# Kernel tuning notes

Hardware: AMD Instinct MI355X
Metric: run time of the kernel (lower is better)

## Reference

```python
import jax, jax.numpy as jnp
import numpy as np

D_MODEL = 1024
N_HEADS = 16
D_HEAD = D_MODEL // N_HEADS
BATCH = 2
SEQ = 2048


def setup_inputs() -> dict:
    key = jax.random.key(0)
    ks = jax.random.split(key, 16)
    s = 0.02
    d = D_MODEL
    return {
        "x": jax.random.normal(ks[0], (BATCH, SEQ, d), jnp.float32),
        "Wq": jax.random.normal(ks[1], (d, d), jnp.float32) * s,
        "bq": jnp.zeros((d,), jnp.float32),
        "Wk": jax.random.normal(ks[2], (d, d), jnp.float32) * s,
        "bk": jnp.zeros((d,), jnp.float32),
        "Wv": jax.random.normal(ks[3], (d, d), jnp.float32) * s,
        "bv": jnp.zeros((d,), jnp.float32),
        "Wo": jax.random.normal(ks[4], (d, d), jnp.float32) * s,
        "bo": jnp.zeros((d,), jnp.float32),
        "Wt": jax.random.normal(ks[5], (d, 1), jnp.float32) * s,
        "bt": jnp.zeros((1,), jnp.float32),
        "Wg": jax.random.normal(ks[6], (d, d), jnp.float32) * s,
        "bg": jnp.zeros((d,), jnp.float32),
    }


def _evolved_attention(x, Wq, bq, Wk, bk, Wv, bv, Wo, bo, Wt, bt, Wg, bg):
    B, S, D = x.shape
    H, dh = N_HEADS, D_HEAD

    def heads(y):  # [B,S,D] -> [B,H,S,dh]
        return y.reshape(B, S, H, dh).transpose(0, 2, 1, 3)

    q = heads(x @ Wq + bq)
    k = heads(x @ Wk + bk)
    v = heads(x @ Wv + bv)

    # cosine similarity (F.normalize with eps=1e-12)
    qn = q / jnp.maximum(jnp.linalg.norm(q, axis=-1, keepdims=True), 1e-12)
    kn = k / jnp.maximum(jnp.linalg.norm(k, axis=-1, keepdims=True), 1e-12)
    scores = jnp.einsum("bhqd,bhkd->bhqk", qn, kn)

    # adaptive temperature: sigmoid(temp_proj(mean_s x)) + 0.5, shape [B,1]
    temp = jax.nn.sigmoid(x.mean(axis=1) @ Wt + bt) + 0.5  # [B,1]
    scores = scores / temp[:, None, None, :]  # broadcast [B,1,1,1]

    # sparsemax-style: softmax over top-k (k = S//4), scattered back
    kk = max(1, S // 4)
    vals, idx = jax.lax.top_k(scores, kk)          # [B,H,S,kk]
    w = jax.nn.softmax(vals, axis=-1)
    rows = jnp.arange(B * H * S)[:, None]
    attn = (
        jnp.zeros((B * H * S, S), scores.dtype)
        .at[rows, idx.reshape(-1, kk)]
        .set(w.reshape(-1, kk))
        .reshape(B, H, S, S)
    )

    out = jnp.einsum("bhqk,bhkd->bhqd", attn, v)
    out = out.transpose(0, 2, 1, 3).reshape(B, S, D)
    out = out @ Wo + bo

    # highway gating
    gate = jax.nn.sigmoid(x @ Wg + bg)
    return gate * out + (1.0 - gate) * x


def reference(x, Wq, bq, Wk, bk, Wv, bv, Wo, bo, Wt, bt, Wg, bg):
    return _evolved_attention(x, Wq, bq, Wk, bk, Wv, bv, Wo, bo, Wt, bt, Wg, bg)
```

## Files before the change

### kernel.cpp

```cpp
#include <hip/hip_runtime.h>

typedef unsigned short u16;
typedef __attribute__((ext_vector_type(4))) float f32x4;
typedef __attribute__((ext_vector_type(8))) short bf16x8;
typedef __attribute__((ext_vector_type(4))) int i32x4;

#define BB 2
#define SS 2048
#define DD 1024
#define HH 16
#define DH 64
#define KK 512

#define OFF_SCAL  ((size_t)0)
#define OFF_WT    ((size_t)256)
#define OFF_XB    (OFF_WT + (size_t)5*1024*1024*2)
#define OFF_AO    OFF_XB
#define OFF_QH    (OFF_XB + (size_t)4096*1024*2)
#define OFF_QN    (OFF_QH + (size_t)4096*4096*2)
#define OFF_KN    (OFF_QN + (size_t)4096*1024*2)
#define OFF_VT    (OFF_KN + (size_t)4096*1024*2)

__device__ __forceinline__ float b2f(u16 u) { return __uint_as_float(((unsigned)u) << 16); }
__device__ __forceinline__ u16 f2b(float f) {
    unsigned u = __float_as_uint(f);
    return (u16)((u + 0x7fffu + ((u >> 16) & 1u)) >> 16);
}

__device__ __forceinline__ void gload16(const u16* g, u16* l) {
    __builtin_amdgcn_global_load_lds(
        (__attribute__((address_space(1))) void*)g,
        (__attribute__((address_space(3))) void*)l, 16, 0, 0);
}

__global__ __launch_bounds__(256) void convert_x(const float* x, u16* xb) {
    int i = (blockIdx.x * 256 + threadIdx.x) * 4;
    float4 v = *(const float4*)(x + i);
    u16 r0 = f2b(v.x), r1 = f2b(v.y), r2 = f2b(v.z), r3 = f2b(v.w);
    xb[i] = r0; xb[i + 1] = r1; xb[i + 2] = r2; xb[i + 3] = r3;
}

__global__ __launch_bounds__(256) void transpose_w(
        const float* Wq, const float* Wk, const float* Wv, const float* Wg, const float* Wo,
        u16* WT) {
    int z = blockIdx.z;
    const float* src = (z == 0) ? Wq : (z == 1) ? Wk : (z == 2) ? Wv : (z == 3) ? Wg : Wo;
    u16* dst = WT + (size_t)z * 1024 * 1024;
    __shared__ float tile[64][65];
    int n0 = blockIdx.x * 64, k0 = blockIdx.y * 64;
    int rbase = threadIdx.x >> 6, c = threadIdx.x & 63;
#pragma unroll
    for (int i = 0; i < 16; i++) {
        int r = i * 4 + rbase;
        tile[r][c] = src[(size_t)(k0 + r) * 1024 + n0 + c];
    }
    __syncthreads();
#pragma unroll
    for (int i = 0; i < 16; i++) {
        int r = i * 4 + rbase;
        dst[(size_t)(n0 + r) * 1024 + k0 + c] = f2b(tile[c][r]);
    }
}

__global__ __launch_bounds__(256) void temp_partial(const float* x, const float* Wt,
                                                    float* accbuf) {
    int b = blockIdx.x >> 5, ch = blockIdx.x & 31;
    float a = 0.f;
    for (int si = 0; si < 64; si++) {
        int s = ch * 64 + si;
        const float* xr = x + ((size_t)(b * SS + s)) * DD;
#pragma unroll
        for (int k = 0; k < 4; k++) {
            int c = threadIdx.x + k * 256;
            a += xr[c] * Wt[c];
        }
    }
    for (int o = 32; o; o >>= 1) a += __shfl_xor(a, o);
    __shared__ float red[4];
    if ((threadIdx.x & 63) == 0) red[threadIdx.x >> 6] = a;
    __syncthreads();
    if (threadIdx.x == 0) atomicAdd(&accbuf[b], red[0] + red[1] + red[2] + red[3]);
}

__global__ void temp_final(const float* accbuf, const float* bt, float* itemp) {
    int t = threadIdx.x;
    if (t < BB) {
        float v = accbuf[t] / (float)SS + bt[0];
        float tmp = 1.f / (1.f + __expf(-v)) + 0.5f;
        itemp[t] = 1.f / tmp;
    }
}

__global__ __launch_bounds__(256) void gemm_qkvg(
        const u16* X, const u16* WT,
        const float* bq, const float* bk, const float* bv, const float* bg, u16* Qh) {
    __shared__ __align__(16) u16 la[128 * 32];
    __shared__ __align__(16) u16 lb[128 * 32];
    int tid = threadIdx.x, wid = tid >> 6, lane = tid & 63;
    int quad = lane >> 4, ml = lane & 15;
    int m0 = blockIdx.x * 128, n0 = blockIdx.y * 128;
    int wr = wid >> 1, wc = wid & 1;

    f32x4 acc[4][4];
#pragma unroll
    for (int i = 0; i < 4; i++)
#pragma unroll
        for (int j = 0; j < 4; j++) acc[i][j] = (f32x4){0.f, 0.f, 0.f, 0.f};

    int t0 = wid * 2, t1 = t0 + 1;
    int r0 = lane >> 2, kp = lane & 3;
    const u16* ga0 = X + (size_t)(m0 + t0 * 16 + r0) * 1024 + kp * 8;
    const u16* ga1 = X + (size_t)(m0 + t1 * 16 + r0) * 1024 + kp * 8;
    const u16* gb0 = WT + (size_t)(n0 + t0 * 16 + r0) * 1024 + kp * 8;
    const u16* gb1 = WT + (size_t)(n0 + t1 * 16 + r0) * 1024 + kp * 8;
    u16* la0 = la + t0 * 512; u16* la1 = la + t1 * 512;
    u16* lb0 = lb + t0 * 512; u16* lb1 = lb + t1 * 512;

    for (int k0 = 0; k0 < 1024; k0 += 32) {
        gload16(ga0 + k0, la0);
        gload16(ga1 + k0, la1);
        gload16(gb0 + k0, lb0);
        gload16(gb1 + k0, lb1);
        __syncthreads();
        bf16x8 af[4], bfr[4];
#pragma unroll
        for (int mi = 0; mi < 4; mi++)
            af[mi] = *(const bf16x8*)&la[(wr * 64 + mi * 16 + ml) * 32 + quad * 8];
#pragma unroll
        for (int ni = 0; ni < 4; ni++)
            bfr[ni] = *(const bf16x8*)&lb[(wc * 64 + ni * 16 + ml) * 32 + quad * 8];
#pragma unroll
        for (int mi = 0; mi < 4; mi++)
#pragma unroll
            for (int ni = 0; ni < 4; ni++)
                acc[mi][ni] = __builtin_amdgcn_mfma_f32_16x16x32_bf16(af[mi], bfr[ni],
                                                                      acc[mi][ni], 0, 0, 0);
        __syncthreads();
    }

#pragma unroll
    for (int mi = 0; mi < 4; mi++)
#pragma unroll
        for (int ni = 0; ni < 4; ni++) {
            int col = n0 + wc * 64 + ni * 16 + ml;
            int mat = col >> 10, bc = col & 1023;
            const float* bp = (mat == 0) ? bq : (mat == 1) ? bk : (mat == 2) ? bv : bg;
            float bias = bp[bc];
#pragma unroll
            for (int r = 0; r < 4; r++) {
                int row = m0 + wr * 64 + mi * 16 + quad * 4 + r;
                Qh[(size_t)row * 4096 + col] = f2b(acc[mi][ni][r] + bias);
            }
        }
}

__global__ __launch_bounds__(256) void norm_repack(const u16* Qh, u16* qn, u16* kn, u16* vt) {
    int wid = threadIdx.x >> 6, lane = threadIdx.x & 63;
    int idx = blockIdx.x * 4 + wid;
    int token = idx >> 4, h = idx & 15;
    int b = token >> 11, s = token & 2047;
    int bh = b * HH + h;
    const u16* rowp = Qh + (size_t)token * 4096 + h * 64;
    float q = b2f(rowp[lane]);
    float k = b2f(rowp[1024 + lane]);
    u16 v = rowp[2048 + lane];
    float sq = q * q, sk = k * k;
    for (int o = 32; o; o >>= 1) { sq += __shfl_xor(sq, o); sk += __shfl_xor(sk, o); }
    float qd = fmaxf(sqrtf(sq), 1e-12f), kd = fmaxf(sqrtf(sk), 1e-12f);
    qn[((size_t)bh * SS + s) * DH + lane] = f2b(q / qd);
    kn[((size_t)bh * SS + s) * DH + lane] = f2b(k / kd);
    vt[((size_t)bh * DH + lane) * SS + s] = v;
}

#define EST 2088

__global__ __launch_bounds__(1024, 8) void attn_kernel(
        const u16* qn, const u16* kn, const u16* vt, const float* itemp, u16* ao) {
    __shared__ __align__(16) u16 e16[16 * EST];
    __shared__ float pvp[3][16][66];
    __shared__ float zrow_s[16];

    int tid = threadIdx.x, wid = tid >> 6, lane = tid & 63;
    int quad = lane >> 4, nl = lane & 15;
    int bid = blockIdx.x;
    int swz = (bid & 7) * 512 + (bid >> 3);
    int bh = swz >> 7, qt = swz & 127;
    int b = bh >> 4, h = bh & 15;
    const u16* qbase = qn + ((size_t)bh * SS + qt * 16) * DH;
    const u16* kbase = kn + (size_t)bh * SS * DH;
    const u16* vbase = vt + (size_t)bh * DH * SS;
    float it = itemp[b];

    bf16x8 aq0 = *(const bf16x8*)(qbase + nl * DH + quad * 8);
    bf16x8 aq1 = *(const bf16x8*)(qbase + nl * DH + 32 + quad * 8);

#pragma unroll 4
    for (int c = 0; c < 8; c++) {
        int j = c * 256 + wid * 16 + nl;
        const u16* kr = kbase + (size_t)j * DH;
        bf16x8 b0 = *(const bf16x8*)(kr + quad * 8);
        bf16x8 b1 = *(const bf16x8*)(kr + 32 + quad * 8);
        f32x4 acc = (f32x4){0.f, 0.f, 0.f, 0.f};
        __builtin_amdgcn_s_setprio(1);
        acc = __builtin_amdgcn_mfma_f32_16x16x32_bf16(aq0, b0, acc, 0, 0, 0);
        acc = __builtin_amdgcn_mfma_f32_16x16x32_bf16(aq1, b1, acc, 0, 0, 0);
        __builtin_amdgcn_s_setprio(0);
#pragma unroll
        for (int r = 0; r < 4; r++) e16[(quad * 4 + r) * EST + j] = f2b(acc[r] * it);
    }
    __syncthreads();

    {
        u16* rp = &e16[wid * EST];
        int kk[32];
#pragma unroll
        for (int i = 0; i < 4; i++) {
            i32x4 kv = *(const i32x4*)(rp + i * 512 + lane * 8);
#pragma unroll
            for (int j = 0; j < 4; j++) {
                unsigned r2 = (unsigned)kv[j];
                unsigned t = ((r2 >> 15) & 0x00010001u) * 0x7FFFu;
                unsigned key2 = r2 ^ 0x80008000u ^ t;
                int lo = (int)(key2 & 0xFFFFu), hi = (int)(key2 >> 16);
                asm volatile("v_mov_b32 %0, %1" : "=v"(kk[i * 8 + j * 2]) : "v"(lo));
                asm volatile("v_mov_b32 %0, %1" : "=v"(kk[i * 8 + j * 2 + 1]) : "v"(hi));
            }
        }

        int P = 0;
        for (int bit = 15; bit >= 0; bit--) {
            int cand = P | (1 << bit);
            int c0 = 0, c1 = 0, c2 = 0, c3 = 0;
#pragma unroll
            for (int c = 0; c < 32; c += 4) {
                c0 += (int)__popcll(__ballot(kk[c] >= cand));
                c1 += (int)__popcll(__ballot(kk[c + 1] >= cand));
                c2 += (int)__popcll(__ballot(kk[c + 2] >= cand));
                c3 += (int)__popcll(__ballot(kk[c + 3] >= cand));
            }
            int cnt = (c0 + c1) + (c2 + c3);
            if (cnt >= KK) P = cand;
            if (cnt == KK) break;
        }

        float z = 0.f;
#pragma unroll
        for (int i = 0; i < 4; i++) {
            i32x4 ev;
#pragma unroll
            for (int j = 0; j < 4; j++) {
                int k0i = kk[i * 8 + j * 2], k1i = kk[i * 8 + j * 2 + 1];
                unsigned r0 = (unsigned)k0i ^ ((k0i & 0x8000) ? 0x8000u : 0xFFFFu);
                unsigned r1 = (unsigned)k1i ^ ((k1i & 0x8000) ? 0x8000u : 0xFFFFu);
                float f0 = __uint_as_float(r0 << 16);
                float f1 = __uint_as_float(r1 << 16);
                float e0 = (k0i >= P) ? __expf(f0) : 0.f;
                float e1 = (k1i >= P) ? __expf(f1) : 0.f;
                z += e0 + e1;
                int pw;
                asm("v_cvt_pk_bf16_f32 %0, %1, %2" : "=v"(pw) : "v"(e0), "v"(e1));
                ev[j] = pw;
            }
            *(i32x4*)(rp + i * 512 + lane * 8) = ev;
        }
#pragma unroll
        for (int o = 32; o; o >>= 1) z += __shfl_xor(z, o);
        if (lane == 0) zrow_s[wid] = z;
    }
    __syncthreads();

    f32x4 accp = (f32x4){0.f, 0.f, 0.f, 0.f};
    int kq = wid >> 2, g = wid & 3;
    int dh = g * 16 + nl;
    const u16* vrow = vbase + (size_t)dh * SS;
#pragma unroll 4
    for (int c = 0; c < 8; c++) {
        int j0 = kq * 512 + c * 64;
#pragma unroll
        for (int ks = 0; ks < 2; ks++) {
            bf16x8 a = *(const bf16x8*)&e16[nl * EST + j0 + ks * 32 + quad * 8];
            bf16x8 bfr = *(const bf16x8*)(vrow + j0 + ks * 32 + quad * 8);
            __builtin_amdgcn_s_setprio(1);
            accp = __builtin_amdgcn_mfma_f32_16x16x32_bf16(a, bfr, accp, 0, 0, 0);
            __builtin_amdgcn_s_setprio(0);
        }
    }
    if (kq) {
#pragma unroll
        for (int r = 0; r < 4; r++) pvp[kq - 1][quad * 4 + r][dh] = accp[r];
    }
    __syncthreads();
    if (kq == 0) {
#pragma unroll
        for (int r = 0; r < 4; r++) {
            int q = quad * 4 + r;
            float val = (accp[r] + pvp[0][q][dh] + pvp[1][q][dh] + pvp[2][q][dh]) / zrow_s[q];
            size_t row = (size_t)(b * SS + qt * 16 + q);
            ao[row * DD + h * 64 + dh] = f2b(val);
        }
    }
}

__global__ __launch_bounds__(256) void gemm_out(
        const u16* AO, const u16* WTo, const float* bo,
        const u16* Qh, const float* x, float* out) {
    __shared__ __align__(16) u16 la[128 * 32];
    __shared__ __align__(16) u16 lb[128 * 32];
    int tid = threadIdx.x, wid = tid >> 6, lane = tid & 63;
    int quad = lane >> 4, ml = lane & 15;
    int m0 = blockIdx.x * 128, n0 = blockIdx.y * 128;
    int wr = wid >> 1, wc = wid & 1;

    f32x4 acc[4][4];
#pragma unroll
    for (int i = 0; i < 4; i++)
#pragma unroll
        for (int j = 0; j < 4; j++) acc[i][j] = (f32x4){0.f, 0.f, 0.f, 0.f};

    int t0 = wid * 2, t1 = t0 + 1;
    int r0 = lane >> 2, kp = lane & 3;
    const u16* ga0 = AO + (size_t)(m0 + t0 * 16 + r0) * 1024 + kp * 8;
    const u16* ga1 = AO + (size_t)(m0 + t1 * 16 + r0) * 1024 + kp * 8;
    const u16* gb0 = WTo + (size_t)(n0 + t0 * 16 + r0) * 1024 + kp * 8;
    const u16* gb1 = WTo + (size_t)(n0 + t1 * 16 + r0) * 1024 + kp * 8;
    u16* la0 = la + t0 * 512; u16* la1 = la + t1 * 512;
    u16* lb0 = lb + t0 * 512; u16* lb1 = lb + t1 * 512;

    for (int k0 = 0; k0 < 1024; k0 += 32) {
        gload16(ga0 + k0, la0);
        gload16(ga1 + k0, la1);
        gload16(gb0 + k0, lb0);
        gload16(gb1 + k0, lb1);
        __syncthreads();
        bf16x8 af[4], bfr[4];
#pragma unroll
        for (int mi = 0; mi < 4; mi++)
            af[mi] = *(const bf16x8*)&la[(wr * 64 + mi * 16 + ml) * 32 + quad * 8];
#pragma unroll
        for (int ni = 0; ni < 4; ni++)
            bfr[ni] = *(const bf16x8*)&lb[(wc * 64 + ni * 16 + ml) * 32 + quad * 8];
#pragma unroll
        for (int mi = 0; mi < 4; mi++)
#pragma unroll
            for (int ni = 0; ni < 4; ni++)
                acc[mi][ni] = __builtin_amdgcn_mfma_f32_16x16x32_bf16(af[mi], bfr[ni],
                                                                      acc[mi][ni], 0, 0, 0);
        __syncthreads();
    }

#pragma unroll
    for (int mi = 0; mi < 4; mi++)
#pragma unroll
        for (int ni = 0; ni < 4; ni++) {
            int col = n0 + wc * 64 + ni * 16 + ml;
            float bias = bo[col];
#pragma unroll
            for (int r = 0; r < 4; r++) {
                int row = m0 + wr * 64 + mi * 16 + quad * 4 + r;
                float gv = b2f(Qh[(size_t)row * 4096 + 3072 + col]);
                float gate = 1.f / (1.f + __expf(-gv));
                float xv = x[(size_t)row * 1024 + col];
                float o = acc[mi][ni][r] + bias;
                out[(size_t)row * 1024 + col] = gate * o + (1.f - gate) * xv;
            }
        }
}

extern "C" void kernel_launch(void* const* d_in, const int* in_sizes, int n_in,
                              void* d_out, int out_size, void* d_ws, size_t ws_size,
                              hipStream_t stream) {
    const float* x  = (const float*)d_in[0];
    const float* Wq = (const float*)d_in[1];
    const float* bq = (const float*)d_in[2];
    const float* Wk = (const float*)d_in[3];
    const float* bk = (const float*)d_in[4];
    const float* Wv = (const float*)d_in[5];
    const float* bv = (const float*)d_in[6];
    const float* Wo = (const float*)d_in[7];
    const float* bo = (const float*)d_in[8];
    const float* Wt = (const float*)d_in[9];
    const float* bt = (const float*)d_in[10];
    const float* Wg = (const float*)d_in[11];
    const float* bg = (const float*)d_in[12];

    char* w = (char*)d_ws;
    float* accbuf = (float*)(w + OFF_SCAL);
    float* itemp  = accbuf + 2;
    u16*   WT     = (u16*)(w + OFF_WT);
    u16*   xb     = (u16*)(w + OFF_XB);
    u16*   ao     = (u16*)(w + OFF_AO);
    u16*   Qh     = (u16*)(w + OFF_QH);
    u16*   qn     = (u16*)(w + OFF_QN);
    u16*   kn     = (u16*)(w + OFF_KN);
    u16*   vt     = (u16*)(w + OFF_VT);

    hipMemsetAsync(accbuf, 0, 2 * sizeof(float), stream);

    convert_x<<<4096, 256, 0, stream>>>(x, xb);
    transpose_w<<<dim3(16, 16, 5), 256, 0, stream>>>(Wq, Wk, Wv, Wg, Wo, WT);
    temp_partial<<<64, 256, 0, stream>>>(x, Wt, accbuf);
    temp_final<<<1, 64, 0, stream>>>(accbuf, bt, itemp);
    gemm_qkvg<<<dim3(32, 32), 256, 0, stream>>>(xb, WT, bq, bk, bv, bg, Qh);
    norm_repack<<<16384, 256, 0, stream>>>(Qh, qn, kn, vt);
    attn_kernel<<<4096, 1024, 0, stream>>>(qn, kn, vt, itemp, ao);
    gemm_out<<<dim3(32, 8), 256, 0, stream>>>(ao, WT + (size_t)4 * 1024 * 1024, bo, Qh, x,
                                              (float*)d_out);
}
```

Baseline: 499.8 us.

## Replace bitwise ballot top-k threshold search with two-pass radix histogram selection

Finds the per-row top-512 threshold with two 8-bit radix histogram passes in shared memory, followed by a wave-level suffix scan. This replaces the earlier 16-iteration bitwise binary search built on ballots. Scores are mapped to a fixed-point 16-bit key, and shared memory is reused between the histogram and the PV partial buffer. The aim is to cut the many ballot/popcount rounds, at the cost of LDS atomic contention and slight quantization of the key ordering.

```diff
diff --git a/kernel.cpp b/kernel.cpp
--- a/kernel.cpp
+++ b/kernel.cpp
@@ -174,10 +174,41 @@
 
 #define EST 2088
 
+struct SelRes { int b; unsigned above; };
+
+__device__ __forceinline__ SelRes suffix_sel(const unsigned* hist, unsigned need, int lane) {
+    unsigned w0 = hist[lane * 2], w1 = hist[lane * 2 + 1];
+    unsigned c0 = w0 & 0xFFFFu, c1 = w0 >> 16, c2 = w1 & 0xFFFFu, c3 = w1 >> 16;
+    unsigned sl = c0 + c1 + c2 + c3;
+    unsigned suf = sl;
+#pragma unroll
+    for (int off = 1; off < 64; off <<= 1) {
+        unsigned t = __shfl_down(suf, off);
+        if (lane + off < 64) suf += t;
+    }
+    unsigned Hh = suf - sl;
+    unsigned s3 = Hh + c3, s2 = s3 + c2, s1 = s2 + c1, s0 = s1 + c0;
+    int cand = (s3 >= need) ? lane * 4 + 3 :
+               (s2 >= need) ? lane * 4 + 2 :
+               (s1 >= need) ? lane * 4 + 1 :
+               (s0 >= need) ? lane * 4 : -1;
+#pragma unroll
+    for (int off = 32; off; off >>= 1) cand = max(cand, __shfl_xor(cand, off));
+    int k = cand & 3;
+    unsigned x = Hh;
+    if (k <= 2) x += c3;
+    if (k <= 1) x += c2;
+    if (k == 0) x += c1;
+    SelRes r;
+    r.b = cand;
+    r.above = __shfl(x, cand >> 2);
+    return r;
+}
+
 __global__ __launch_bounds__(1024, 8) void attn_kernel(
         const u16* qn, const u16* kn, const u16* vt, const float* itemp, u16* ao) {
     __shared__ __align__(16) u16 e16[16 * EST];
-    __shared__ float pvp[3][16][66];
+    __shared__ __align__(16) char smem2[12672];
     __shared__ float zrow_s[16];
 
     int tid = threadIdx.x, wid = tid >> 6, lane = tid & 63;
@@ -212,50 +243,63 @@
 
     {
         u16* rp = &e16[wid * EST];
-        int kk[32];
+        unsigned* hist = reinterpret_cast<unsigned*>(smem2) + wid * 128;
+        const float SC = 16000.0f, OF = 32768.0f;
+
+        hist[lane] = 0u; hist[64 + lane] = 0u;
 #pragma unroll
         for (int i = 0; i < 4; i++) {
             i32x4 kv = *(const i32x4*)(rp + i * 512 + lane * 8);
 #pragma unroll
             for (int j = 0; j < 4; j++) {
                 unsigned r2 = (unsigned)kv[j];
-                unsigned t = ((r2 >> 15) & 0x00010001u) * 0x7FFFu;
-                unsigned key2 = r2 ^ 0x80008000u ^ t;
-                int lo = (int)(key2 & 0xFFFFu), hi = (int)(key2 >> 16);
-                asm volatile("v_mov_b32 %0, %1" : "=v"(kk[i * 8 + j * 2]) : "v"(lo));
-                asm volatile("v_mov_b32 %0, %1" : "=v"(kk[i * 8 + j * 2 + 1]) : "v"(hi));
+                unsigned u0 = (unsigned)fmaf(__uint_as_float(r2 << 16), SC, OF);
+                unsigned u1 = (unsigned)fmaf(__uint_as_float(r2 & 0xFFFF0000u), SC, OF);
+                unsigned b0i = u0 >> 8, b1i = u1 >> 8;
+                atomicAdd(&hist[b0i >> 1], 1u << ((b0i & 1) * 16));
+                atomicAdd(&hist[b1i >> 1], 1u << ((b1i & 1) * 16));
             }
         }
-
-        int P = 0;
-        for (int bit = 15; bit >= 0; bit--) {
-            int cand = P | (1 << bit);
-            int c0 = 0, c1 = 0, c2 = 0, c3 = 0;
-#pragma unroll
-            for (int c = 0; c < 32; c += 4) {
-                c0 += (int)__popcll(__ballot(kk[c] >= cand));
-                c1 += (int)__popcll(__ballot(kk[c + 1] >= cand));
-                c2 += (int)__popcll(__ballot(kk[c + 2] >= cand));
-                c3 += (int)__popcll(__ballot(kk[c + 3] >= cand));
+        SelRes hiSel = suffix_sel(hist, (unsigned)KK, lane);
+        int B0 = hiSel.b;
+        unsigned need2 = (unsigned)KK - hiSel.above;
+
+        hist[lane] = 0u; hist[64 + lane] = 0u;
+#pragma unroll
+        for (int i = 0; i < 4; i++) {
+            i32x4 kv = *(const i32x4*)(rp + i * 512 + lane * 8);
+#pragma unroll
+            for (int j = 0; j < 4; j++) {
+                unsigned r2 = (unsigned)kv[j];
+                unsigned u0 = (unsigned)fmaf(__uint_as_float(r2 << 16), SC, OF);
+                unsigned u1 = (unsigned)fmaf(__uint_as_float(r2 & 0xFFFF0000u), SC, OF);
+                if ((int)(u0 >> 8) == B0) {
+                    unsigned l0 = u0 & 255u;
+                    atomicAdd(&hist[l0 >> 1], 1u << ((l0 & 1) * 16));
+                }
+                if ((int)(u1 >> 8) == B0) {
+                    unsigned l1 = u1 & 255u;
+                    atomicAdd(&hist[l1 >> 1], 1u << ((l1 & 1) * 16));
+                }
             }
-            int cnt = (c0 + c1) + (c2 + c3);
-            if (cnt >= KK) P = cand;
-            if (cnt == KK) break;
-        }
+        }
+        SelRes loSel = suffix_sel(hist, need2, lane);
+        unsigned P = ((unsigned)B0 << 8) | (unsigned)loSel.b;
 
         float z = 0.f;
 #pragma unroll
         for (int i = 0; i < 4; i++) {
+            i32x4 kv = *(const i32x4*)(rp + i * 512 + lane * 8);
             i32x4 ev;
 #pragma unroll
             for (int j = 0; j < 4; j++) {
-                int k0i = kk[i * 8 + j * 2], k1i = kk[i * 8 + j * 2 + 1];
-                unsigned r0 = (unsigned)k0i ^ ((k0i & 0x8000) ? 0x8000u : 0xFFFFu);
-                unsigned r1 = (unsigned)k1i ^ ((k1i & 0x8000) ? 0x8000u : 0xFFFFu);
-                float f0 = __uint_as_float(r0 << 16);
-                float f1 = __uint_as_float(r1 << 16);
-                float e0 = (k0i >= P) ? __expf(f0) : 0.f;
-                float e1 = (k1i >= P) ? __expf(f1) : 0.f;
+                unsigned r2 = (unsigned)kv[j];
+                float f0 = __uint_as_float(r2 << 16);
+                float f1 = __uint_as_float(r2 & 0xFFFF0000u);
+                unsigned u0 = (unsigned)fmaf(f0, SC, OF);
+                unsigned u1 = (unsigned)fmaf(f1, SC, OF);
+                float e0 = (u0 >= P) ? __expf(f0) : 0.f;
+                float e1 = (u1 >= P) ? __expf(f1) : 0.f;
                 z += e0 + e1;
                 int pw;
                 asm("v_cvt_pk_bf16_f32 %0, %1, %2" : "=v"(pw) : "v"(e0), "v"(e1));
@@ -269,6 +313,7 @@
     }
     __syncthreads();
 
+    float (*pvp)[16][66] = reinterpret_cast<float(*)[16][66]>(smem2);
     f32x4 accp = (f32x4){0.f, 0.f, 0.f, 0.f};
     int kq = wid >> 2, g = wid & 3;
     int dh = g * 16 + nl;
```

New measurement: 500.7 us. About the same (+0.2%).
